# Performance work log

Measured on AMD Instinct MI355X. Metric: run time of the kernel, lower is better.

Reference implementation:

```python
import jax, jax.numpy as jnp
import numpy as np

BN_EPS = 1e-5

def knn_indices(loc, new_loc, k):
    # squared distances [B, M, N] via ||y||^2 + ||x||^2 - 2 y.x (no [B,M,N,3] materialization)
    x2 = jnp.sum(loc * loc, axis=-1)          # [B, N]
    y2 = jnp.sum(new_loc * new_loc, axis=-1)  # [B, M]
    d2 = y2[:, :, None] + x2[:, None, :] - 2.0 * jnp.einsum('bmc,bnc->bmn', new_loc, loc)
    _, idx = jax.lax.top_k(-d2, k)            # smallest-k -> [B, M, K]
    return idx

def gather_neighbors(x, idx):
    # x [B, N, C], idx [B, M, K] -> [B, M, K, C]
    return jax.vmap(lambda xb, ib: xb[ib])(x, idx)

def conv_bn_relu(x, W, g, b):
    # x [B, Cin, M, K]; 1x1 conv (no bias) + training-mode BatchNorm2d + ReLU
    y = jnp.einsum('oc,bcmk->bomk', W, x)
    mu = jnp.mean(y, axis=(0, 2, 3), keepdims=True)
    var = jnp.var(y, axis=(0, 2, 3), keepdims=True)  # biased, as torch BN uses for normalization
    y = (y - mu) * jax.lax.rsqrt(var + BN_EPS)
    return jax.nn.relu(y * g[None, :, None, None] + b[None, :, None, None])

def setup_inputs() -> dict:
    key = jax.random.key(0)
    ks = jax.random.split(key, 8)
    B, N, M, C = 16, 4096, 1024, 64
    loc = jax.random.normal(ks[0], (B, N, 3), dtype=jnp.float32)
    new_loc = jax.random.normal(ks[1], (B, M, 3), dtype=jnp.float32)
    features = jax.random.normal(ks[2], (B, C, N), dtype=jnp.float32)
    W1 = jax.random.normal(ks[3], (64, 67), dtype=jnp.float32) * (1.0 / np.sqrt(67.0))
    W2 = jax.random.normal(ks[4], (64, 64), dtype=jnp.float32) * (1.0 / np.sqrt(64.0))
    W3 = jax.random.normal(ks[5], (128, 64), dtype=jnp.float32) * (1.0 / np.sqrt(64.0))
    return {
        'loc': loc, 'new_loc': new_loc, 'features': features,
        'W1': W1, 'g1': jnp.ones(64, jnp.float32), 'b1': jnp.zeros(64, jnp.float32),
        'W2': W2, 'g2': jnp.ones(64, jnp.float32), 'b2': jnp.zeros(64, jnp.float32),
        'W3': W3, 'g3': jnp.ones(128, jnp.float32), 'b3': jnp.zeros(128, jnp.float32),
    }

def reference(loc, new_loc, features, W1, g1, b1, W2, g2, b2, W3, g3, b3):
    K = 32
    idx = knn_indices(loc, new_loc, K)                      # [B, M, K]
    knn_loc = gather_neighbors(loc, idx)                    # [B, M, K, 3]
    knn_loc = jnp.transpose(knn_loc, (0, 3, 1, 2))          # [B, 3, M, K]
    knn_loc = knn_loc - jnp.transpose(new_loc, (0, 2, 1))[..., None]  # relative xyz
    knn_feat = gather_neighbors(jnp.transpose(features, (0, 2, 1)), idx)  # [B, M, K, C]
    knn_feat = jnp.transpose(knn_feat, (0, 3, 1, 2))        # [B, C, M, K]
    h = jnp.concatenate([knn_loc, knn_feat], axis=1)        # [B, C+3, M, K]
    h = conv_bn_relu(h, W1, g1, b1)
    h = conv_bn_relu(h, W2, g2, b2)
    h = conv_bn_relu(h, W3, g3, b3)
    return jnp.max(h, axis=3)                               # [B, 128, M]
```

## Files before the change

kernel.cpp:

```cpp
#include <hip/hip_runtime.h>
#include <stdint.h>

#define B_   16
#define N_   4096
#define M_   1024
#define NT   (B_*M_*32)
#define BM   (B_*M_)
#define REP  64

typedef unsigned short u16;
typedef unsigned long long u64;
typedef __attribute__((ext_vector_type(8))) short short8;
typedef __attribute__((ext_vector_type(4))) float f32x4;

union FragU { uint4 u; short8 s; };

__device__ __forceinline__ float bf2f(u16 u){
    return __uint_as_float(((unsigned int)u) << 16);
}
__device__ __forceinline__ u16 f2bf(float f){
    unsigned int u = __float_as_uint(f);
    return (u16)((u + 0x7FFFu + ((u >> 16) & 1u)) >> 16);
}

__global__ __launch_bounds__(256) void k_feat(const float* __restrict__ feat,
                                              float* __restrict__ featT){
    __shared__ float tile[64][65];
    int b  = blockIdx.y;
    int n0 = blockIdx.x * 64;
    for (int t = threadIdx.x; t < 4096; t += 256){
        int c = t >> 6, n = t & 63;
        tile[c][n] = feat[((size_t)(b*64 + c))*N_ + n0 + n];
    }
    __syncthreads();
    for (int t = threadIdx.x; t < 4096; t += 256){
        int n = t >> 6, c = t & 63;
        featT[((size_t)(b*N_) + n0 + n)*64 + c] = tile[c][n];
    }
}

__global__ __launch_bounds__(256) void k_prep(const float* __restrict__ locF,
                                              float4* __restrict__ locP){
    int i = blockIdx.x*256 + threadIdx.x;
    float lx = locF[(size_t)i*3+0], ly = locF[(size_t)i*3+1], lz = locF[(size_t)i*3+2];
    float x2 = __fadd_rn(__fadd_rn(__fmul_rn(lx,lx), __fmul_rn(ly,ly)), __fmul_rn(lz,lz));
    locP[i] = make_float4(lx, ly, lz, x2);
}

__global__ __launch_bounds__(256) void k_knn(const float4* __restrict__ locP,
                                             const float* __restrict__ nlocF,
                                             int* __restrict__ idxOut){
    const int tid  = threadIdx.x;
    const int lane = tid & 63, wv = tid >> 6;
    const int q    = blockIdx.x;
    const int b    = q >> 10, m = q & 1023;

    float qx = nlocF[(size_t)(b*M_ + m)*3 + 0];
    float qy = nlocF[(size_t)(b*M_ + m)*3 + 1];
    float qz = nlocF[(size_t)(b*M_ + m)*3 + 2];
    float y2 = __fadd_rn(__fadd_rn(__fmul_rn(qx,qx), __fmul_rn(qy,qy)), __fmul_rn(qz,qz));

    unsigned int key[16];
    const float4* lb = locP + (size_t)b*N_;
    #pragma unroll
    for (int i = 0; i < 16; ++i){
        int n = i*256 + tid;
        float4 p = lb[n];
        float dt = __fadd_rn(__fadd_rn(__fmul_rn(qx,p.x), __fmul_rn(qy,p.y)), __fmul_rn(qz,p.z));
        float d2 = __fsub_rn(__fadd_rn(y2, p.w), __fmul_rn(2.0f, dt));
        d2 = fmaxf(d2, 0.0f);
        key[i] = __float_as_uint(d2);
    }

    __shared__ unsigned int hist[4][256];
    __shared__ float wmm[4][2];
    __shared__ u64 cand[128];
    __shared__ int sOut[32];
    __shared__ int outCnt, candCnt;

    float lmin = 3.4e38f, lmax = 0.0f;
    #pragma unroll
    for (int i = 0; i < 16; ++i){
        float kf = __uint_as_float(key[i]);
        lmin = fminf(lmin, kf); lmax = fmaxf(lmax, kf);
    }
    #pragma unroll
    for (int st = 1; st < 64; st <<= 1){
        lmin = fminf(lmin, __shfl_xor(lmin, st, 64));
        lmax = fmaxf(lmax, __shfl_xor(lmax, st, 64));
    }
    if (tid == 0){ outCnt = 0; candCnt = 0; }
    if (lane == 0){ wmm[wv][0] = lmin; wmm[wv][1] = lmax; }
    __syncthreads();
    float lo = fminf(fminf(wmm[0][0], wmm[1][0]), fminf(wmm[2][0], wmm[3][0]));
    float hi = fmaxf(fmaxf(wmm[0][1], wmm[1][1]), fmaxf(wmm[2][1], wmm[3][1]));

    unsigned int act = 0xFFFFu;
    int bkt[16];
    int R = 32;

    for (int lvl = 0; lvl < 8; ++lvl){
        float scale = 255.0f / fmaxf(hi - lo, 1e-35f);
        ((uint4*)hist)[tid] = make_uint4(0,0,0,0);
        __syncthreads();
        #pragma unroll
        for (int i = 0; i < 16; ++i){
            if (act & (1u << i)){
                float kf = __uint_as_float(key[i]);
                int bb = (int)((kf - lo) * scale);
                bb = bb < 0 ? 0 : (bb > 255 ? 255 : bb);
                bkt[i] = bb;
                atomicAdd(&hist[wv][bb], 1u);
            }
        }
        __syncthreads();
        uint4 ha = *(const uint4*)&hist[0][lane << 2];
        uint4 hb = *(const uint4*)&hist[1][lane << 2];
        uint4 hc = *(const uint4*)&hist[2][lane << 2];
        uint4 hd = *(const uint4*)&hist[3][lane << 2];
        uint4 h = make_uint4(ha.x+hb.x+hc.x+hd.x, ha.y+hb.y+hc.y+hd.y,
                             ha.z+hb.z+hc.z+hd.z, ha.w+hb.w+hc.w+hd.w);
        int tot = (int)(h.x + h.y + h.z + h.w);
        int v = tot;
        #pragma unroll
        for (int st = 1; st < 64; st <<= 1){
            int u = __shfl_up(v, st, 64);
            if (lane >= st) v += u;
        }
        u64 bal = __ballot(v >= R);
        int Ls = __ffsll((unsigned long long)bal) - 1;
        int exclS = __shfl(v - tot, Ls, 64);
        int hx = __shfl((int)h.x, Ls, 64), hy = __shfl((int)h.y, Ls, 64);
        int hz = __shfl((int)h.z, Ls, 64), hw = __shfl((int)h.w, Ls, 64);
        int c0 = exclS + hx, c1 = c0 + hy, c2 = c1 + hz;
        int jj    = (c0 >= R) ? 0 : (c1 >= R) ? 1 : (c2 >= R) ? 2 : 3;
        int below = (jj == 0) ? exclS : (jj == 1) ? c0 : (jj == 2) ? c1 : c2;
        int cnt   = (jj == 0) ? hx : (jj == 1) ? hy : (jj == 2) ? hz : hw;
        int qb = Ls*4 + jj;
        R -= below;
        bool brk = (cnt <= 128) || (lvl == 7);

        float nlo = 3.4e38f, nhi = 0.0f;
        #pragma unroll
        for (int i = 0; i < 16; ++i){
            if (act & (1u << i)){
                int bb = bkt[i];
                if (bb < qb){
                    int pos = atomicAdd(&outCnt, 1);
                    if (pos < 32) sOut[pos] = i*256 + tid;
                    act &= ~(1u << i);
                } else if (bb > qb){
                    act &= ~(1u << i);
                } else if (!brk){
                    float kf = __uint_as_float(key[i]);
                    nlo = fminf(nlo, kf); nhi = fmaxf(nhi, kf);
                }
            }
        }
        if (brk) break;
        #pragma unroll
        for (int st = 1; st < 64; st <<= 1){
            nlo = fminf(nlo, __shfl_xor(nlo, st, 64));
            nhi = fmaxf(nhi, __shfl_xor(nhi, st, 64));
        }
        __syncthreads();
        if (lane == 0){ wmm[wv][0] = nlo; wmm[wv][1] = nhi; }
        __syncthreads();
        lo = fminf(fminf(wmm[0][0], wmm[1][0]), fminf(wmm[2][0], wmm[3][0]));
        hi = fmaxf(fmaxf(wmm[0][1], wmm[1][1]), fmaxf(wmm[2][1], wmm[3][1]));
    }

    #pragma unroll
    for (int i = 0; i < 16; ++i){
        if (act & (1u << i)){
            int pos = atomicAdd(&candCnt, 1);
            if (pos < 128) cand[pos] = (((u64)key[i]) << 32) | (unsigned int)(i*256 + tid);
        }
    }
    __syncthreads();
    int c = candCnt < 128 ? candCnt : 128;
    int base = outCnt;
    if (tid < c){
        u64 me = cand[tid];
        int rank = 0;
        for (int j = 0; j < c; ++j) rank += (cand[j] < me) ? 1 : 0;
        if (rank < R) sOut[base + rank] = (int)(me & 0xFFFFFFFFull);
    }
    __syncthreads();
    if (tid < 32) idxOut[(size_t)q*32 + tid] = sOut[tid];
}

__global__ __launch_bounds__(256) void k_conv1m(const int* __restrict__ idx,
                                                const float* __restrict__ locF,
                                                const float* __restrict__ nlocF,
                                                const float* __restrict__ featT,
                                                const float* __restrict__ W1,
                                                u16* __restrict__ y1,
                                                float* __restrict__ gsum,
                                                float* __restrict__ gsq){
    __shared__ uint4 bfB[4*5*64];
    __shared__ u16  tileT[64*136];
    __shared__ float sSum[64], sSq[64];
    const int t   = threadIdx.x;
    const int bid = blockIdx.x;
    const int rep = bid & (REP-1);
    const int swz = (bid & 7)*512 + (bid >> 3);
    const int s0  = swz * 128;
    const int b   = s0 >> 15;

    if (t < 64){ sSum[t] = 0.0f; sSq[t] = 0.0f; }

    #pragma unroll
    for (int rp = 0; rp < 5; ++rp){
        int cid = rp*256 + t;
        int ln  = cid & 63;
        int kk  = (cid >> 6) % 5;
        int nt  = cid / 320;
        int o   = nt*16 + (ln & 15);
        int qq  = ln >> 4;
        int cb  = kk*16 + qq*4;
        unsigned int d[4];
        #pragma unroll
        for (int h = 0; h < 4; ++h){
            int c = cb + h;
            float wv = (c < 64) ? W1[o*67 + 3 + c] : ((c < 67) ? W1[o*67 + (c - 64)] : 0.0f);
            unsigned int wh = (unsigned int)f2bf(wv);
            d[h] = wh | (wh << 16);
        }
        bfB[cid] = make_uint4(d[0], d[1], d[2], d[3]);
    }

    const int w = t >> 6, lane = t & 63;
    const int m15 = lane & 15, q = lane >> 4;

    int nrow[2], sg[2];
    float4 fa[2][4];
    #pragma unroll
    for (int mt = 0; mt < 2; ++mt){
        int sl = (2*w + mt)*16 + m15;
        sg[mt] = s0 + sl;
        int n = idx[sg[mt]]; if ((unsigned)n >= N_) n = 0;
        nrow[mt] = n;
        const float4* fp = (const float4*)&featT[((size_t)(b*N_) + n)*64];
        #pragma unroll
        for (int kq = 0; kq < 4; ++kq)
            fa[mt][kq] = fp[kq*4 + q];
    }
    uint4 axyz[2];
    axyz[0] = make_uint4(0,0,0,0); axyz[1] = make_uint4(0,0,0,0);
    if (q == 0){
        #pragma unroll
        for (int mt = 0; mt < 2; ++mt){
            int n = nrow[mt];
            int m = (sg[mt] >> 5) & 1023;
            const float* lp = &locF[(size_t)(b*N_ + n)*3];
            const float* qp = &nlocF[(size_t)(b*M_ + m)*3];
            unsigned int dd[3];
            #pragma unroll
            for (int e = 0; e < 3; ++e){
                float r  = lp[e] - qp[e];
                u16 hi   = f2bf(r);
                float lo = r - bf2f(hi);
                dd[e] = (unsigned int)hi | (((unsigned int)f2bf(lo)) << 16);
            }
            axyz[mt] = make_uint4(dd[0], dd[1], dd[2], 0u);
        }
    }
    __syncthreads();

    f32x4 acc[2][4];
    #pragma unroll
    for (int mt = 0; mt < 2; ++mt)
        #pragma unroll
        for (int nt = 0; nt < 4; ++nt)
            acc[mt][nt] = (f32x4){0.0f, 0.0f, 0.0f, 0.0f};

    #pragma unroll
    for (int kk = 0; kk < 5; ++kk){
        FragU af[2];
        #pragma unroll
        for (int mt = 0; mt < 2; ++mt){
            if (kk < 4){
                float4 f = fa[mt][kk];
                float fv[4] = {f.x, f.y, f.z, f.w};
                unsigned int d[4];
                #pragma unroll
                for (int e = 0; e < 4; ++e){
                    u16 hi   = f2bf(fv[e]);
                    float lo = fv[e] - bf2f(hi);
                    d[e] = (unsigned int)hi | (((unsigned int)f2bf(lo)) << 16);
                }
                af[mt].u = make_uint4(d[0], d[1], d[2], d[3]);
            } else {
                af[mt].u = axyz[mt];
            }
        }
        #pragma unroll
        for (int nt = 0; nt < 4; ++nt){
            FragU bu; bu.u = bfB[(nt*5 + kk)*64 + lane];
            #pragma unroll
            for (int mt = 0; mt < 2; ++mt)
                acc[mt][nt] = __builtin_amdgcn_mfma_f32_16x16x32_bf16(af[mt].s, bu.s, acc[mt][nt], 0, 0, 0);
        }
    }

    {
        float st4[4], sq4[4];
        #pragma unroll
        for (int nt = 0; nt < 4; ++nt){ st4[nt] = 0.0f; sq4[nt] = 0.0f; }
        #pragma unroll
        for (int mt = 0; mt < 2; ++mt)
            #pragma unroll
            for (int nt = 0; nt < 4; ++nt){
                f32x4 a = acc[mt][nt];
                st4[nt] += (a[0] + a[1]) + (a[2] + a[3]);
                float qv = a[0]*a[0];
                qv = fmaf(a[1], a[1], qv); qv = fmaf(a[2], a[2], qv); qv = fmaf(a[3], a[3], qv);
                sq4[nt] += qv;
            }
        #pragma unroll
        for (int st = 16; st < 64; st <<= 1){
            #pragma unroll
            for (int nt = 0; nt < 4; ++nt){
                st4[nt] += __shfl_xor(st4[nt], st, 64);
                sq4[nt] += __shfl_xor(sq4[nt], st, 64);
            }
        }
        if (lane < 16){
            #pragma unroll
            for (int nt = 0; nt < 4; ++nt){
                atomicAdd(&sSum[nt*16 + lane], st4[nt]);
                atomicAdd(&sSq[nt*16 + lane],  sq4[nt]);
            }
        }
    }

    #pragma unroll
    for (int mt = 0; mt < 2; ++mt){
        int s_base = w*32 + mt*16 + (lane >> 4)*4;
        #pragma unroll
        for (int nt = 0; nt < 4; ++nt){
            int o = nt*16 + (lane & 15);
            f32x4 a = acc[mt][nt];
            unsigned int p01 = (unsigned int)f2bf(a[0]) | (((unsigned int)f2bf(a[1])) << 16);
            unsigned int p23 = (unsigned int)f2bf(a[2]) | (((unsigned int)f2bf(a[3])) << 16);
            *(unsigned int*)&tileT[o*136 + s_base]     = p01;
            *(unsigned int*)&tileT[o*136 + s_base + 2] = p23;
        }
    }
    __syncthreads();

    {
        int c  = t >> 2;
        int g0 = (t & 3)*32;
        #pragma unroll
        for (int j = 0; j < 4; ++j){
            uint4 v = *(const uint4*)&tileT[c*136 + g0 + j*8];
            *(uint4*)&y1[(size_t)c*NT + s0 + g0 + j*8] = v;
        }
    }
    if (t < 64){
        atomicAdd(&gsum[rep*64 + t], sSum[t]);
        atomicAdd(&gsq[rep*64 + t],  sSq[t]);
    }
}

__global__ __launch_bounds__(256) void k_conv2m(const u16* __restrict__ yin,
                                                const float* __restrict__ W2,
                                                const float* __restrict__ prm,
                                                u16* __restrict__ yout,
                                                float* __restrict__ gsum,
                                                float* __restrict__ gsq){
    __shared__ uint4 bfA[2048];
    __shared__ uint4 bfB[512];
    __shared__ u16  tileT[64*264];
    __shared__ float sS[64], sT[64];
    __shared__ float sSum[64], sSq[64];
    const int t   = threadIdx.x;
    const int rep = blockIdx.x & (REP-1);
    const int s0  = blockIdx.x * 256;

    if (t < 64){ sS[t] = prm[t]; sT[t] = prm[64 + t]; sSum[t] = 0.0f; sSq[t] = 0.0f; }
    __syncthreads();

    #pragma unroll
    for (int rp = 0; rp < 2; ++rp){
        int cid = rp*256 + t;
        int ln  = cid & 63;
        int kk  = (cid >> 6) & 1;
        int nt  = cid >> 7;
        int o   = nt*16 + (ln & 15);
        int k0  = kk*32 + (ln >> 4)*8;
        const float* wp = &W2[o*64 + k0];
        unsigned int d[4];
        #pragma unroll
        for (int h = 0; h < 4; ++h)
            d[h] = (unsigned int)f2bf(wp[2*h]) | (((unsigned int)f2bf(wp[2*h+1])) << 16);
        bfB[cid] = make_uint4(d[0], d[1], d[2], d[3]);
    }

    {
        int oct = t >> 5;
        int sg  = t & 31;
        int c0  = oct*8;
        int kk  = oct >> 2;
        int qd  = oct & 3;
        u16 rb[8][8];
        #pragma unroll
        for (int j = 0; j < 8; ++j){
            int c = c0 + j;
            uint4 pk = *(const uint4*)&yin[(size_t)c*NT + s0 + sg*8];
            float sc = sS[c], tb = sT[c];
            unsigned int w4[4] = {pk.x, pk.y, pk.z, pk.w};
            #pragma unroll
            for (int h = 0; h < 4; ++h){
                rb[j][2*h]   = f2bf(fmaxf(fmaf(bf2f((u16)(w4[h] & 0xFFFF)), sc, tb), 0.0f));
                rb[j][2*h+1] = f2bf(fmaxf(fmaf(bf2f((u16)(w4[h] >> 16)),   sc, tb), 0.0f));
            }
        }
        #pragma unroll
        for (int i = 0; i < 8; ++i){
            int s   = sg*8 + i;
            int mtg = s >> 4, m15 = s & 15;
            int l64 = qd*16 + m15;
            int cb  = (mtg*2 + kk)*64 + (l64 ^ (mtg & 7));
            unsigned int d[4];
            #pragma unroll
            for (int h = 0; h < 4; ++h)
                d[h] = (unsigned int)rb[2*h][i] | (((unsigned int)rb[2*h+1][i]) << 16);
            bfA[cb] = make_uint4(d[0], d[1], d[2], d[3]);
        }
    }
    __syncthreads();

    const int w = t >> 6, lane = t & 63;
    f32x4 acc[4][4];
    #pragma unroll
    for (int mt = 0; mt < 4; ++mt)
        #pragma unroll
        for (int nt = 0; nt < 4; ++nt)
            acc[mt][nt] = (f32x4){0.0f, 0.0f, 0.0f, 0.0f};

    #pragma unroll
    for (int kk = 0; kk < 2; ++kk){
        short8 af[4];
        #pragma unroll
        for (int mt = 0; mt < 4; ++mt){
            int tile = 4*w + mt;
            af[mt] = *((const short8*)&bfA[(tile*2 + kk)*64 + (lane ^ (tile & 7))]);
        }
        #pragma unroll
        for (int nt = 0; nt < 4; ++nt){
            short8 bfr = *((const short8*)&bfB[(nt*2 + kk)*64 + lane]);
            #pragma unroll
            for (int mt = 0; mt < 4; ++mt)
                acc[mt][nt] = __builtin_amdgcn_mfma_f32_16x16x32_bf16(af[mt], bfr, acc[mt][nt], 0, 0, 0);
        }
    }

    {
        float st4[4], sq4[4];
        #pragma unroll
        for (int nt = 0; nt < 4; ++nt){ st4[nt] = 0.0f; sq4[nt] = 0.0f; }
        #pragma unroll
        for (int mt = 0; mt < 4; ++mt)
            #pragma unroll
            for (int nt = 0; nt < 4; ++nt){
                f32x4 a = acc[mt][nt];
                st4[nt] += (a[0] + a[1]) + (a[2] + a[3]);
                float qq = a[0]*a[0];
                qq = fmaf(a[1], a[1], qq); qq = fmaf(a[2], a[2], qq); qq = fmaf(a[3], a[3], qq);
                sq4[nt] += qq;
            }
        #pragma unroll
        for (int st = 16; st < 64; st <<= 1){
            #pragma unroll
            for (int nt = 0; nt < 4; ++nt){
                st4[nt] += __shfl_xor(st4[nt], st, 64);
                sq4[nt] += __shfl_xor(sq4[nt], st, 64);
            }
        }
        if (lane < 16){
            #pragma unroll
            for (int nt = 0; nt < 4; ++nt){
                atomicAdd(&sSum[nt*16 + lane], st4[nt]);
                atomicAdd(&sSq[nt*16 + lane],  sq4[nt]);
            }
        }
    }

    #pragma unroll
    for (int mt = 0; mt < 4; ++mt){
        int s_base = w*64 + mt*16 + (lane >> 4)*4;
        #pragma unroll
        for (int nt = 0; nt < 4; ++nt){
            int o = nt*16 + (lane & 15);
            f32x4 a = acc[mt][nt];
            unsigned int p01 = (unsigned int)f2bf(a[0]) | (((unsigned int)f2bf(a[1])) << 16);
            unsigned int p23 = (unsigned int)f2bf(a[2]) | (((unsigned int)f2bf(a[3])) << 16);
            *(unsigned int*)&tileT[o*264 + s_base]     = p01;
            *(unsigned int*)&tileT[o*264 + s_base + 2] = p23;
        }
    }
    __syncthreads();

    {
        int c  = t >> 2;
        int g0 = (t & 3)*8;
        #pragma unroll
        for (int j = 0; j < 8; ++j){
            uint4 v = *(const uint4*)&tileT[c*264 + (g0 + j)*8];
            *(uint4*)&yout[(size_t)c*NT + s0 + (g0 + j)*8] = v;
        }
    }
    if (t < 64){
        atomicAdd(&gsum[rep*64 + t], sSum[t]);
        atomicAdd(&gsq[rep*64 + t],  sSq[t]);
    }
}

__global__ __launch_bounds__(256) void k_conv3m(const u16* __restrict__ yin,
                                                const float* __restrict__ W3,
                                                const float* __restrict__ prm,
                                                float* __restrict__ gsum, float* __restrict__ gsq,
                                                float* __restrict__ gmax, float* __restrict__ gmin){
    __shared__ uint4 bfA[2048];
    __shared__ uint4 bfB[1024];
    __shared__ float sS[64], sT[64];
    __shared__ float sSum[128], sSq[128];
    const int t   = threadIdx.x;
    const int rep = blockIdx.x & (REP-1);
    const int s0  = blockIdx.x * 256;

    if (t < 64){ sS[t] = prm[t]; sT[t] = prm[64 + t]; }
    if (t < 128){ sSum[t] = 0.0f; sSq[t] = 0.0f; }
    __syncthreads();

    #pragma unroll
    for (int rp = 0; rp < 4; ++rp){
        int cid = rp*256 + t;
        int ln  = cid & 63;
        int kk  = (cid >> 6) & 1;
        int nt  = cid >> 7;
        int o   = nt*16 + (ln & 15);
        int k0  = kk*32 + (ln >> 4)*8;
        const float* wp = &W3[o*64 + k0];
        unsigned int d[4];
        #pragma unroll
        for (int h = 0; h < 4; ++h)
            d[h] = (unsigned int)f2bf(wp[2*h]) | (((unsigned int)f2bf(wp[2*h+1])) << 16);
        bfB[cid] = make_uint4(d[0], d[1], d[2], d[3]);
    }

    {
        int oct = t >> 5;
        int sg  = t & 31;
        int c0  = oct*8;
        int kk  = oct >> 2;
        int qd  = oct & 3;
        u16 rb[8][8];
        #pragma unroll
        for (int j = 0; j < 8; ++j){
            int c = c0 + j;
            uint4 pk = *(const uint4*)&yin[(size_t)c*NT + s0 + sg*8];
            float sc = sS[c], tb = sT[c];
            unsigned int w4[4] = {pk.x, pk.y, pk.z, pk.w};
            #pragma unroll
            for (int h = 0; h < 4; ++h){
                rb[j][2*h]   = f2bf(fmaxf(fmaf(bf2f((u16)(w4[h] & 0xFFFF)), sc, tb), 0.0f));
                rb[j][2*h+1] = f2bf(fmaxf(fmaf(bf2f((u16)(w4[h] >> 16)),   sc, tb), 0.0f));
            }
        }
        #pragma unroll
        for (int i = 0; i < 8; ++i){
            int s   = sg*8 + i;
            int mtg = s >> 4, m15 = s & 15;
            int l64 = qd*16 + m15;
            int cb  = (mtg*2 + kk)*64 + (l64 ^ (mtg & 7));
            unsigned int d[4];
            #pragma unroll
            for (int h = 0; h < 4; ++h)
                d[h] = (unsigned int)rb[2*h][i] | (((unsigned int)rb[2*h+1][i]) << 16);
            bfA[cb] = make_uint4(d[0], d[1], d[2], d[3]);
        }
    }
    __syncthreads();

    const int w = t >> 6, lane = t & 63;
    f32x4 acc[4][8];
    #pragma unroll
    for (int mt = 0; mt < 4; ++mt)
        #pragma unroll
        for (int nt = 0; nt < 8; ++nt)
            acc[mt][nt] = (f32x4){0.0f, 0.0f, 0.0f, 0.0f};

    #pragma unroll
    for (int kk = 0; kk < 2; ++kk){
        short8 af[4];
        #pragma unroll
        for (int mt = 0; mt < 4; ++mt){
            int tile = 4*w + mt;
            af[mt] = *((const short8*)&bfA[(tile*2 + kk)*64 + (lane ^ (tile & 7))]);
        }
        #pragma unroll
        for (int nt = 0; nt < 8; ++nt){
            short8 bfr = *((const short8*)&bfB[(nt*2 + kk)*64 + lane]);
            #pragma unroll
            for (int mt = 0; mt < 4; ++mt)
                acc[mt][nt] = __builtin_amdgcn_mfma_f32_16x16x32_bf16(af[mt], bfr, acc[mt][nt], 0, 0, 0);
        }
    }

    float stS[8], stQ[8];
    #pragma unroll
    for (int nt = 0; nt < 8; ++nt){ stS[nt] = 0.0f; stQ[nt] = 0.0f; }

    #pragma unroll
    for (int g = 0; g < 2; ++g){
        const size_t gg = (size_t)(blockIdx.x*8 + w*2 + g);
        #pragma unroll
        for (int nt = 0; nt < 8; ++nt){
            f32x4 a0 = acc[2*g][nt], a1 = acc[2*g+1][nt];
            float mx = fmaxf(fmaxf(fmaxf(a0[0], a0[1]), fmaxf(a0[2], a0[3])),
                             fmaxf(fmaxf(a1[0], a1[1]), fmaxf(a1[2], a1[3])));
            float mn = fminf(fminf(fminf(a0[0], a0[1]), fminf(a0[2], a0[3])),
                             fminf(fminf(a1[0], a1[1]), fminf(a1[2], a1[3])));
            float sm = (a0[0]+a0[1]) + (a0[2]+a0[3]) + (a1[0]+a1[1]) + (a1[2]+a1[3]);
            float sq = a0[0]*a0[0];
            sq = fmaf(a0[1], a0[1], sq); sq = fmaf(a0[2], a0[2], sq); sq = fmaf(a0[3], a0[3], sq);
            sq = fmaf(a1[0], a1[0], sq); sq = fmaf(a1[1], a1[1], sq); sq = fmaf(a1[2], a1[2], sq);
            sq = fmaf(a1[3], a1[3], sq);
            #pragma unroll
            for (int st = 16; st < 64; st <<= 1){
                mx = fmaxf(mx, __shfl_xor(mx, st, 64));
                mn = fminf(mn, __shfl_xor(mn, st, 64));
                sm += __shfl_xor(sm, st, 64);
                sq += __shfl_xor(sq, st, 64);
            }
            if (lane < 16){
                gmax[gg*128 + nt*16 + lane] = mx;
                gmin[gg*128 + nt*16 + lane] = mn;
            }
            stS[nt] += sm; stQ[nt] += sq;
        }
    }
    if (lane < 16){
        #pragma unroll
        for (int nt = 0; nt < 8; ++nt){
            atomicAdd(&sSum[nt*16 + lane], stS[nt]);
            atomicAdd(&sSq[nt*16 + lane],  stQ[nt]);
        }
    }
    __syncthreads();
    if (t < 128){
        atomicAdd(&gsum[rep*128 + t], sSum[t]);
        atomicAdd(&gsq[rep*128 + t],  sSq[t]);
    }
}

__global__ void k_fold(const float* __restrict__ sum, const float* __restrict__ sumsq,
                       const float* __restrict__ gW, const float* __restrict__ bW,
                       float* __restrict__ prm, int C){
    int c = threadIdx.x;
    if (c < C){
        float s = 0.0f, q = 0.0f;
        for (int r = 0; r < REP; ++r){
            s += sum[r*C + c];
            q += sumsq[r*C + c];
        }
        const float inv = 1.0f / (float)NT;
        float mu  = s * inv;
        float var = q * inv - mu*mu;
        float sc  = gW[c] / sqrtf(var + 1e-5f);
        prm[c]     = sc;
        prm[C + c] = bW[c] - mu*sc;
    }
}

__global__ __launch_bounds__(256) void k_final(const float* __restrict__ gmax,
                                               const float* __restrict__ gmin,
                                               const float* __restrict__ prm,
                                               float* __restrict__ out){
    __shared__ float tile[32][129];
    __shared__ float sS[128], sT[128];
    const int t   = threadIdx.x;
    const int blk = blockIdx.x;
    const int b   = blk >> 5;
    const int m0  = (blk & 31) * 32;
    if (t < 128){ sS[t] = prm[t]; sT[t] = prm[128 + t]; }
    __syncthreads();
    #pragma unroll
    for (int i = 0; i < 16; ++i){
        int v  = i*256 + t;
        int ml = v >> 7, o = v & 127;
        float sc = sS[o];
        size_t gi = (size_t)(b*M_ + m0 + ml)*128 + o;
        float val = (sc >= 0.0f) ? gmax[gi] : gmin[gi];
        tile[ml][o] = fmaxf(fmaf(val, sc, sT[o]), 0.0f);
    }
    __syncthreads();
    #pragma unroll
    for (int i = 0; i < 16; ++i){
        int v  = i*256 + t;
        int o  = v >> 5, ml = v & 31;
        out[((size_t)(b*128 + o))*M_ + m0 + ml] = tile[ml][o];
    }
}

extern "C" void kernel_launch(void* const* d_in, const int* in_sizes, int n_in,
                              void* d_out, int out_size, void* d_ws, size_t ws_size,
                              hipStream_t stream){
    const float* loc  = (const float*)d_in[0];
    const float* nloc = (const float*)d_in[1];
    const float* feat = (const float*)d_in[2];
    const float* W1   = (const float*)d_in[3];
    const float* g1   = (const float*)d_in[4];
    const float* b1   = (const float*)d_in[5];
    const float* W2   = (const float*)d_in[6];
    const float* g2   = (const float*)d_in[7];
    const float* b2   = (const float*)d_in[8];
    const float* W3   = (const float*)d_in[9];
    const float* g3   = (const float*)d_in[10];
    const float* b3   = (const float*)d_in[11];
    float* out = (float*)d_out;

    char* ws = (char*)d_ws;
    float* prm1  = (float*)(ws + 2048);
    float* prm2  = (float*)(ws + 2048 + 512);
    float* prm3  = (float*)(ws + 2048 + 1024);
    int*   idx   = (int*)(ws + 4096);
    float* gmax  = (float*)(ws + 2101248);
    float* gmin  = (float*)(ws + 10489856);
    float* featT = (float*)(ws + 18878464);
    u16*   y1    = (u16*)(ws + 35655680);
    u16*   y2    = (u16*)(ws + 102764544);
    float4* locP = (float4*)gmax;
    float* rep12 = (float*)(ws + 2101248 + 1048576);
    float* sum1 = rep12;
    float* sq1  = rep12 + REP*64;
    float* sum2 = rep12 + 2*REP*64;
    float* sq2  = rep12 + 3*REP*64;
    float* rep3 = (float*)featT;
    float* sum3 = rep3;
    float* sq3  = rep3 + REP*128;

    hipMemsetAsync(rep12, 0, 4*REP*64*sizeof(float), stream);

    k_feat<<<dim3(N_/64, B_), 256, 0, stream>>>(feat, featT);
    k_prep<<<(B_*N_)/256, 256, 0, stream>>>(loc, locP);
    k_knn<<<B_*M_, 256, 0, stream>>>(locP, nloc, idx);

    k_conv1m<<<NT/128, 256, 0, stream>>>(idx, loc, nloc, featT, W1, y1, sum1, sq1);
    k_fold<<<1, 128, 0, stream>>>(sum1, sq1, g1, b1, prm1, 64);
    hipMemsetAsync(rep3, 0, 2*REP*128*sizeof(float), stream);

    k_conv2m<<<NT/256, 256, 0, stream>>>(y1, W2, prm1, y2, sum2, sq2);
    k_fold<<<1, 128, 0, stream>>>(sum2, sq2, g2, b2, prm2, 64);

    k_conv3m<<<NT/256, 256, 0, stream>>>(y2, W3, prm2, sum3, sq3, gmax, gmin);
    k_fold<<<1, 128, 0, stream>>>(sum3, sq3, g3, b3, prm3, 128);

    k_final<<<dim3(B_*32), 256, 0, stream>>>(gmax, gmin, prm3, out);
}
```

Before: 369.5 us.

## Make KNN radix-select per-wavefront, then merge four wave top-32 lists

Each wavefront now owns a contiguous 1024-point slice and runs its own histogram-based top-32 selection with wave-private shared histograms and candidate buffers. This removes the block-wide __syncthreads barriers and cross-wave min/max exchanges on every refinement level. A final single barrier merges the four per-wave 32-entry lists by rank counting over 128 keys. The trade-off is four times as many selections over fewer elements each, plus an extra 128-way merge step.

```diff
diff --git a/kernel.cpp b/kernel.cpp
--- a/kernel.cpp
+++ b/kernel.cpp
@@ -55,45 +55,40 @@
     const int q    = blockIdx.x;
     const int b    = q >> 10, m = q & 1023;
 
+    __shared__ unsigned int hist[4][256];
+    __shared__ u64 wOut[4][32];
+    __shared__ u64 wCand[4][128];
+    __shared__ int wCnt[4], wCandN[4];
+
+    if (lane == 0){ wCnt[wv] = 0; wCandN[wv] = 0; }
+
     float qx = nlocF[(size_t)(b*M_ + m)*3 + 0];
     float qy = nlocF[(size_t)(b*M_ + m)*3 + 1];
     float qz = nlocF[(size_t)(b*M_ + m)*3 + 2];
     float y2 = __fadd_rn(__fadd_rn(__fmul_rn(qx,qx), __fmul_rn(qy,qy)), __fmul_rn(qz,qz));
 
     unsigned int key[16];
-    const float4* lb = locP + (size_t)b*N_;
+    const float4* lb = locP + (size_t)b*N_ + (size_t)wv*1024;
     #pragma unroll
     for (int i = 0; i < 16; ++i){
-        int n = i*256 + tid;
-        float4 p = lb[n];
+        float4 p = lb[i*64 + lane];
         float dt = __fadd_rn(__fadd_rn(__fmul_rn(qx,p.x), __fmul_rn(qy,p.y)), __fmul_rn(qz,p.z));
         float d2 = __fsub_rn(__fadd_rn(y2, p.w), __fmul_rn(2.0f, dt));
         d2 = fmaxf(d2, 0.0f);
         key[i] = __float_as_uint(d2);
     }
 
-    __shared__ unsigned int hist[4][256];
-    __shared__ float wmm[4][2];
-    __shared__ u64 cand[128];
-    __shared__ int sOut[32];
-    __shared__ int outCnt, candCnt;
-
-    float lmin = 3.4e38f, lmax = 0.0f;
+    float lo = 3.4e38f, hi = 0.0f;
     #pragma unroll
     for (int i = 0; i < 16; ++i){
         float kf = __uint_as_float(key[i]);
-        lmin = fminf(lmin, kf); lmax = fmaxf(lmax, kf);
+        lo = fminf(lo, kf); hi = fmaxf(hi, kf);
     }
     #pragma unroll
     for (int st = 1; st < 64; st <<= 1){
-        lmin = fminf(lmin, __shfl_xor(lmin, st, 64));
-        lmax = fmaxf(lmax, __shfl_xor(lmax, st, 64));
-    }
-    if (tid == 0){ outCnt = 0; candCnt = 0; }
-    if (lane == 0){ wmm[wv][0] = lmin; wmm[wv][1] = lmax; }
-    __syncthreads();
-    float lo = fminf(fminf(wmm[0][0], wmm[1][0]), fminf(wmm[2][0], wmm[3][0]));
-    float hi = fmaxf(fmaxf(wmm[0][1], wmm[1][1]), fmaxf(wmm[2][1], wmm[3][1]));
+        lo = fminf(lo, __shfl_xor(lo, st, 64));
+        hi = fmaxf(hi, __shfl_xor(hi, st, 64));
+    }
 
     unsigned int act = 0xFFFFu;
     int bkt[16];
@@ -101,8 +96,7 @@
 
     for (int lvl = 0; lvl < 8; ++lvl){
         float scale = 255.0f / fmaxf(hi - lo, 1e-35f);
-        ((uint4*)hist)[tid] = make_uint4(0,0,0,0);
-        __syncthreads();
+        *(uint4*)&hist[wv][lane << 2] = make_uint4(0,0,0,0);
         #pragma unroll
         for (int i = 0; i < 16; ++i){
             if (act & (1u << i)){
@@ -113,13 +107,7 @@
                 atomicAdd(&hist[wv][bb], 1u);
             }
         }
-        __syncthreads();
-        uint4 ha = *(const uint4*)&hist[0][lane << 2];
-        uint4 hb = *(const uint4*)&hist[1][lane << 2];
-        uint4 hc = *(const uint4*)&hist[2][lane << 2];
-        uint4 hd = *(const uint4*)&hist[3][lane << 2];
-        uint4 h = make_uint4(ha.x+hb.x+hc.x+hd.x, ha.y+hb.y+hc.y+hd.y,
-                             ha.z+hb.z+hc.z+hd.z, ha.w+hb.w+hc.w+hd.w);
+        uint4 h = *(const uint4*)&hist[wv][lane << 2];
         int tot = (int)(h.x + h.y + h.z + h.w);
         int v = tot;
         #pragma unroll
@@ -146,8 +134,9 @@
             if (act & (1u << i)){
                 int bb = bkt[i];
                 if (bb < qb){
-                    int pos = atomicAdd(&outCnt, 1);
-                    if (pos < 32) sOut[pos] = i*256 + tid;
+                    int pos = atomicAdd(&wCnt[wv], 1);
+                    if (pos < 32)
+                        wOut[wv][pos] = (((u64)key[i]) << 32) | (unsigned int)(wv*1024 + i*64 + lane);
                     act &= ~(1u << i);
                 } else if (bb > qb){
                     act &= ~(1u << i);
@@ -163,31 +152,35 @@
             nlo = fminf(nlo, __shfl_xor(nlo, st, 64));
             nhi = fmaxf(nhi, __shfl_xor(nhi, st, 64));
         }
-        __syncthreads();
-        if (lane == 0){ wmm[wv][0] = nlo; wmm[wv][1] = nhi; }
-        __syncthreads();
-        lo = fminf(fminf(wmm[0][0], wmm[1][0]), fminf(wmm[2][0], wmm[3][0]));
-        hi = fmaxf(fmaxf(wmm[0][1], wmm[1][1]), fmaxf(wmm[2][1], wmm[3][1]));
+        lo = nlo; hi = nhi;
     }
 
     #pragma unroll
     for (int i = 0; i < 16; ++i){
         if (act & (1u << i)){
-            int pos = atomicAdd(&candCnt, 1);
-            if (pos < 128) cand[pos] = (((u64)key[i]) << 32) | (unsigned int)(i*256 + tid);
-        }
-    }
-    __syncthreads();
-    int c = candCnt < 128 ? candCnt : 128;
-    int base = outCnt;
-    if (tid < c){
-        u64 me = cand[tid];
+            int pos = atomicAdd(&wCandN[wv], 1);
+            if (pos < 128)
+                wCand[wv][pos] = (((u64)key[i]) << 32) | (unsigned int)(wv*1024 + i*64 + lane);
+        }
+    }
+    {
+        int cW   = wCandN[wv]; cW = cW < 128 ? cW : 128;
+        int base = wCnt[wv];   base = base < 32 ? base : 32;
+        for (int e = lane; e < cW; e += 64){
+            u64 me = wCand[wv][e];
+            int rank = 0;
+            for (int j = 0; j < cW; ++j) rank += (wCand[wv][j] < me) ? 1 : 0;
+            if (rank < R) wOut[wv][base + rank] = me;
+        }
+    }
+    __syncthreads();
+    if (tid < 128){
+        u64 me = ((const u64*)wOut)[tid];
         int rank = 0;
-        for (int j = 0; j < c; ++j) rank += (cand[j] < me) ? 1 : 0;
-        if (rank < R) sOut[base + rank] = (int)(me & 0xFFFFFFFFull);
-    }
-    __syncthreads();
-    if (tid < 32) idxOut[(size_t)q*32 + tid] = sOut[tid];
+        #pragma unroll 4
+        for (int j = 0; j < 128; ++j) rank += (((const u64*)wOut)[j] < me) ? 1 : 0;
+        if (rank < 32) idxOut[(size_t)q*32 + rank] = (int)(me & 0xFFFFFFFFull);
+    }
 }
 
 __global__ __launch_bounds__(256) void k_conv1m(const int* __restrict__ idx,
```

Result: slower. 397.7 us (+7.6%).
